# Optimization experiments

Measured on AMD Instinct MI355X. Metric: run time of the kernel, lower is better.

Reference implementation:

```python
import jax, jax.numpy as jnp
import numpy as np

N, L, D = 32768, 15, 256
VOCAB, SCORE_MAX = 27, 100


def setup_inputs() -> dict:
    key = jax.random.key(0)
    ks = jax.random.split(key, 16)
    inp = {
        'words': jax.random.randint(ks[0], (N, L), 0, VOCAB, dtype=jnp.int32),
        'rows': jax.random.randint(ks[1], (N,), 0, L, dtype=jnp.int32),
        'cols': jax.random.randint(ks[2], (N,), 0, L, dtype=jnp.int32),
        'dirs': jax.random.randint(ks[3], (N,), 0, 2, dtype=jnp.int32),
        'scores': jax.random.randint(ks[4], (N,), 0, 150, dtype=jnp.int32),
        'letter_emb': jax.random.normal(ks[5], (VOCAB, D), jnp.float32),
        'positional': jax.random.normal(ks[6], (L, D), jnp.float32),
        'Wq': jax.random.normal(ks[7], (D, D), jnp.float32) / np.sqrt(D),
        'bq': jax.random.normal(ks[8], (D,), jnp.float32) * 0.01,
        'Wk': jax.random.normal(ks[9], (D, D), jnp.float32) / np.sqrt(D),
        'bk': jax.random.normal(ks[10], (D,), jnp.float32) * 0.01,
        'Wv': jax.random.normal(ks[11], (D, D), jnp.float32) / np.sqrt(D),
        'bv': jax.random.normal(ks[12], (D,), jnp.float32) * 0.01,
        'row_emb': jax.random.normal(ks[13], (L, D), jnp.float32),
        'col_emb': jax.random.normal(ks[14], (L, D), jnp.float32),
        'dir_emb': jax.random.normal(ks[15], (2, D), jnp.float32),
        'score_emb': jax.random.normal(jax.random.fold_in(key, 99), (SCORE_MAX, D), jnp.float32),
    }
    return inp


def reference(words, rows, cols, dirs, scores, letter_emb, positional, Wq, bq, Wk, bk, Wv, bv, row_emb, col_emb, dir_emb, score_emb):
    # WordEncoder: letter embedding + positional, then single-head self-attention, sum over positions
    emb = letter_emb[words] + positional[None, :, :]            # [N, L, D]
    q = emb @ Wq.T + bq                                          # [N, L, D]
    k = emb @ Wk.T + bk
    v = emb @ Wv.T + bv
    att = jax.nn.softmax(jnp.einsum('nld,nmd->nlm', q, k), axis=-1)  # [N, L, L]
    word = jnp.einsum('nlm,nmd->nd', att, v)                     # (att @ v).sum(axis=1) -> [N, D]
    # VectorEncoder
    vector = row_emb[rows] + col_emb[cols] + dir_emb[dirs]       # [N, D]
    # score embedding (clamped to score_max - 1)
    score_v = score_emb[jnp.minimum(scores, SCORE_MAX - 1)]      # [N, D]
    # original computes word_enc(move.word) twice (word + ordered) -> 2 * word
    return 2.0 * word + vector + score_v
```

## Files before the change

kernel.cpp:

```cpp
#include <hip/hip_runtime.h>
#include <hip/hip_bf16.h>

#define NMOV 32768
#define LW 15
#define DIM 256
#define NVOC 27
#define NR 405
#define GSH 408
#define MPB 16

__device__ __forceinline__ float b2f(unsigned short u) {
    return __uint_as_float(((unsigned int)u) << 16);
}

__device__ const unsigned char PAIR_LUT[120] = {
    0x00,
    0x10,0x11,
    0x20,0x21,0x22,
    0x30,0x31,0x32,0x33,
    0x40,0x41,0x42,0x43,0x44,
    0x50,0x51,0x52,0x53,0x54,0x55,
    0x60,0x61,0x62,0x63,0x64,0x65,0x66,
    0x70,0x71,0x72,0x73,0x74,0x75,0x76,0x77,
    0x80,0x81,0x82,0x83,0x84,0x85,0x86,0x87,0x88,
    0x90,0x91,0x92,0x93,0x94,0x95,0x96,0x97,0x98,0x99,
    0xA0,0xA1,0xA2,0xA3,0xA4,0xA5,0xA6,0xA7,0xA8,0xA9,0xAA,
    0xB0,0xB1,0xB2,0xB3,0xB4,0xB5,0xB6,0xB7,0xB8,0xB9,0xBA,0xBB,
    0xC0,0xC1,0xC2,0xC3,0xC4,0xC5,0xC6,0xC7,0xC8,0xC9,0xCA,0xCB,0xCC,
    0xD0,0xD1,0xD2,0xD3,0xD4,0xD5,0xD6,0xD7,0xD8,0xD9,0xDA,0xDB,0xDC,0xDD,
    0xE0,0xE1,0xE2,0xE3,0xE4,0xE5,0xE6,0xE7,0xE8,0xE9,0xEA,0xEB,0xEC,0xED,0xEE
};

__global__ __launch_bounds__(256) void qkv_gemm(
    const float* __restrict__ le, const float* __restrict__ pos,
    const float* __restrict__ Wq, const float* __restrict__ bq,
    const float* __restrict__ Wk, const float* __restrict__ bk,
    const float* __restrict__ Wv, const float* __restrict__ bv,
    float* __restrict__ QT, float* __restrict__ KT,
    __hip_bfloat16* __restrict__ VT)
{
    __shared__ float Ash[32][260];
    __shared__ float Bsh[256][69];
    const int t  = threadIdx.x;
    const int gx = blockIdx.x % 12;
    const int gy = blockIdx.x / 12;
    const int r0 = gy * 32;
    const int mat = gx >> 2;
    const int nb  = (gx & 3) * 64;
    const float* W  = (mat == 0) ? Wq : (mat == 1) ? Wk : Wv;
    const float* bb = (mat == 0) ? bq : (mat == 1) ? bk : bv;

    #pragma unroll
    for (int s = 0; s < 8; ++s) {
        int slot = s * 256 + t;
        int row = slot >> 6, q4 = slot & 63;
        int r = r0 + row;
        float4 v = make_float4(0.f, 0.f, 0.f, 0.f);
        if (r < NR) {
            int c = r / 15, l = r - c * 15;
            float4 lv = *(const float4*)&le[c * DIM + q4 * 4];
            float4 pv = *(const float4*)&pos[l * DIM + q4 * 4];
            v = make_float4(lv.x + pv.x, lv.y + pv.y, lv.z + pv.z, lv.w + pv.w);
        }
        *(float4*)&Ash[row][q4 * 4] = v;
    }
    #pragma unroll
    for (int s = 0; s < 16; ++s) {
        int slot = s * 256 + t;
        int row = slot >> 6, q4 = slot & 63;
        float4 w4 = *(const float4*)&W[(nb + row) * DIM + q4 * 4];
        Bsh[q4 * 4 + 0][row] = w4.x;
        Bsh[q4 * 4 + 1][row] = w4.y;
        Bsh[q4 * 4 + 2][row] = w4.z;
        Bsh[q4 * 4 + 3][row] = w4.w;
    }
    __syncthreads();

    const int tn = t & 63, tm = t >> 6;
    float acc[8];
    #pragma unroll
    for (int rr = 0; rr < 8; ++rr) acc[rr] = 0.f;

    #pragma unroll 4
    for (int kq = 0; kq < 64; ++kq) {
        float4 a4[8];
        #pragma unroll
        for (int rr = 0; rr < 8; ++rr)
            a4[rr] = *(const float4*)&Ash[tm * 8 + rr][kq * 4];
        float b0 = Bsh[kq * 4 + 0][tn];
        float b1 = Bsh[kq * 4 + 1][tn];
        float b2 = Bsh[kq * 4 + 2][tn];
        float b3 = Bsh[kq * 4 + 3][tn];
        #pragma unroll
        for (int rr = 0; rr < 8; ++rr)
            acc[rr] += a4[rr].x * b0 + a4[rr].y * b1 + a4[rr].z * b2 + a4[rr].w * b3;
    }

    const float bias = bb[nb + tn];
    const int dcol = nb + tn;
    #pragma unroll
    for (int rr = 0; rr < 8; ++rr) {
        int r = r0 + tm * 8 + rr;
        if (r < NR) {
            float v = acc[rr] + bias;
            if (mat == 0)      QT[r * DIM + dcol] = v;
            else if (mat == 1) KT[r * DIM + dcol] = v;
            else               VT[r * DIM + dcol] = __float2bfloat16(v);
        }
    }
}

__global__ __launch_bounds__(256) void h_matrix(
    const float* __restrict__ QT, const float* __restrict__ KT,
    float2* __restrict__ H)
{
    __shared__ float Qi[16][68], Ki[16][68], Qj[16][68], Kj[16][68];

    int rem = blockIdx.x, bi = 0, cnt = 26;
    while (rem >= cnt) { rem -= cnt; ++bi; --cnt; }
    const int bj = bi + rem;
    const int i0 = bi * 16, j0 = bj * 16;
    const int t = threadIdx.x;
    const int ti = t >> 4, tj = t & 15;

    float acc_ij = 0.f, acc_ji = 0.f;

    for (int k0 = 0; k0 < DIM; k0 += 64) {
        #pragma unroll
        for (int s = 0; s < 4; ++s) {
            int slot = s * 256 + t;
            int tile = slot >> 8;
            int r    = (slot >> 4) & 15;
            int c4   = slot & 15;
            int grow = (tile < 2) ? (i0 + r) : (j0 + r);
            const float* src = (tile == 0 || tile == 2) ? QT : KT;
            float4 v = (grow < NR)
                ? *(const float4*)&src[grow * DIM + k0 + c4 * 4]
                : make_float4(0.f, 0.f, 0.f, 0.f);
            float* dst = (tile == 0) ? &Qi[r][c4 * 4]
                       : (tile == 1) ? &Ki[r][c4 * 4]
                       : (tile == 2) ? &Qj[r][c4 * 4] : &Kj[r][c4 * 4];
            *(float4*)dst = v;
        }
        __syncthreads();
        #pragma unroll 4
        for (int k = 0; k < 64; k += 4) {
            float4 qi = *(const float4*)&Qi[ti][k];
            float4 kj = *(const float4*)&Kj[tj][k];
            float4 qj = *(const float4*)&Qj[ti][k];
            float4 ki = *(const float4*)&Ki[tj][k];
            acc_ij += qi.x * kj.x + qi.y * kj.y + qi.z * kj.z + qi.w * kj.w;
            acc_ji += qj.x * ki.x + qj.y * ki.y + qj.z * ki.z + qj.w * ki.w;
        }
        __syncthreads();
    }

    Qi[ti][tj] = acc_ij;
    Ki[ti][tj] = acc_ji;
    __syncthreads();
    const float t_ij = Qi[tj][ti];
    const float t_ji = Ki[tj][ti];

    const int i1 = i0 + ti, j1 = j0 + tj;
    if (i1 < NR && j1 < NR) H[i1 * GSH + j1] = make_float2(acc_ij, t_ji);
    const int i2 = j0 + ti, j2 = i0 + tj;
    if (i2 < NR && j2 < NR) H[i2 * GSH + j2] = make_float2(acc_ji, t_ij);
}

__global__ __launch_bounds__(256) void moves_kernel(
    const int* __restrict__ words, const int* __restrict__ rowsI,
    const int* __restrict__ colsI, const int* __restrict__ dirsI,
    const int* __restrict__ scoresI,
    const float2* __restrict__ H, const __hip_bfloat16* __restrict__ VT,
    const float* __restrict__ row_emb, const float* __restrict__ col_emb,
    const float* __restrict__ dir_emb, const float* __restrict__ score_emb,
    float* __restrict__ out)
{
    __shared__ float S[MPB][LW][17];
    __shared__ int   rIdx[MPB][16];
    __shared__ float csum[MPB][16];
    const int base = blockIdx.x * MPB;
    const int t  = threadIdx.x;
    const int w  = t >> 6;
    const int ln = t & 63;
    const int hw = t >> 5;
    const int j  = t & 31;

    if (ln < 60) {
        int mvl = ln / 15, row = ln - mvl * 15;
        int mv = w * 4 + mvl;
        rIdx[mv][row] = words[(base + mv) * LW + row] * LW + row;
    }
    __builtin_amdgcn_wave_barrier();

    const int mv0 = hw * 2, mv1 = mv0 + 1;
    float2 h0[4], h1[4];
    int ll[4], mm[4];
    #pragma unroll
    for (int k = 0; k < 4; ++k) {
        int p = j + 32 * k;
        if (p < 120) {
            int lm = PAIR_LUT[p];
            ll[k] = lm >> 4; mm[k] = lm & 15;
            h0[k] = H[(size_t)rIdx[mv0][ll[k]] * GSH + rIdx[mv0][mm[k]]];
            h1[k] = H[(size_t)rIdx[mv1][ll[k]] * GSH + rIdx[mv1][mm[k]]];
        }
    }
    #pragma unroll
    for (int k = 0; k < 4; ++k) {
        int p = j + 32 * k;
        if (p < 120) {
            S[mv0][ll[k]][mm[k]] = h0[k].x;
            S[mv0][mm[k]][ll[k]] = h0[k].y;
            S[mv1][ll[k]][mm[k]] = h1[k].x;
            S[mv1][mm[k]][ll[k]] = h1[k].y;
        }
    }
    __builtin_amdgcn_wave_barrier();

    if (ln < 60) {
        int mvl = ln / 15, row = ln - mvl * 15;
        int mv = w * 4 + mvl;
        float s[LW];
        #pragma unroll
        for (int m = 0; m < LW; ++m) s[m] = S[mv][row][m];
        float mx = s[0];
        #pragma unroll
        for (int m = 1; m < LW; ++m) mx = fmaxf(mx, s[m]);
        float sum = 0.f;
        #pragma unroll
        for (int m = 0; m < LW; ++m) { s[m] = __expf(s[m] - mx); sum += s[m]; }
        float inv = 1.0f / sum;
        #pragma unroll
        for (int m = 0; m < LW; ++m) S[mv][row][m] = s[m] * inv;
    }
    __builtin_amdgcn_wave_barrier();

    if (ln < 60) {
        int mvl = ln / 15, col = ln - mvl * 15;
        int mv = w * 4 + mvl;
        float acc = 0.f;
        #pragma unroll
        for (int l = 0; l < LW; ++l) acc += S[mv][l][col];
        csum[mv][col] = acc;
    }
    __builtin_amdgcn_wave_barrier();

    const int d0 = ln * 4;
    const unsigned short* VT16 = (const unsigned short*)VT;
    #pragma unroll 1
    for (int s2 = 0; s2 < 4; ++s2) {
        const int i = w * 4 + s2;
        const int n = base + i;
        float4 re = *(const float4*)&row_emb[rowsI[n] * DIM + d0];
        float4 ce = *(const float4*)&col_emb[colsI[n] * DIM + d0];
        float4 de = *(const float4*)&dir_emb[dirsI[n] * DIM + d0];
        float4 se = *(const float4*)&score_emb[min(scoresI[n], 99) * DIM + d0];
        ushort4 va[8];
        #pragma unroll
        for (int m = 0; m < 8; ++m)
            va[m] = *(const ushort4*)(VT16 + (size_t)rIdx[i][m] * DIM + d0);
        float wx = 0.f, wy = 0.f, wz = 0.f, ww = 0.f;
        #pragma unroll
        for (int m = 0; m < 8; ++m) {
            float c = csum[i][m];
            wx += c * b2f(va[m].x); wy += c * b2f(va[m].y);
            wz += c * b2f(va[m].z); ww += c * b2f(va[m].w);
        }
        ushort4 vb[7];
        #pragma unroll
        for (int m = 0; m < 7; ++m)
            vb[m] = *(const ushort4*)(VT16 + (size_t)rIdx[i][8 + m] * DIM + d0);
        #pragma unroll
        for (int m = 0; m < 7; ++m) {
            float c = csum[i][8 + m];
            wx += c * b2f(vb[m].x); wy += c * b2f(vb[m].y);
            wz += c * b2f(vb[m].z); ww += c * b2f(vb[m].w);
        }
        float4 res;
        res.x = 2.f * wx + re.x + ce.x + de.x + se.x;
        res.y = 2.f * wy + re.y + ce.y + de.y + se.y;
        res.z = 2.f * wz + re.z + ce.z + de.z + se.z;
        res.w = 2.f * ww + re.w + ce.w + de.w + se.w;
        *(float4*)&out[(size_t)n * DIM + d0] = res;
    }
}

extern "C" void kernel_launch(void* const* d_in, const int* in_sizes, int n_in,
                              void* d_out, int out_size, void* d_ws, size_t ws_size,
                              hipStream_t stream)
{
    const int*   words      = (const int*)d_in[0];
    const int*   rowsI      = (const int*)d_in[1];
    const int*   colsI      = (const int*)d_in[2];
    const int*   dirsI      = (const int*)d_in[3];
    const int*   scoresI    = (const int*)d_in[4];
    const float* letter_emb = (const float*)d_in[5];
    const float* positional = (const float*)d_in[6];
    const float* Wq         = (const float*)d_in[7];
    const float* bq         = (const float*)d_in[8];
    const float* Wk         = (const float*)d_in[9];
    const float* bk         = (const float*)d_in[10];
    const float* Wv         = (const float*)d_in[11];
    const float* bv         = (const float*)d_in[12];
    const float* row_emb    = (const float*)d_in[13];
    const float* col_emb    = (const float*)d_in[14];
    const float* dir_emb    = (const float*)d_in[15];
    const float* score_emb  = (const float*)d_in[16];
    float* out = (float*)d_out;

    float*  QT = (float*)d_ws;
    float*  KT = QT + NR * DIM;
    float2* Hm = (float2*)(KT + NR * DIM);
    __hip_bfloat16* VT = (__hip_bfloat16*)((char*)Hm + (size_t)NR * GSH * sizeof(float2));

    qkv_gemm<<<156, 256, 0, stream>>>(letter_emb, positional, Wq, bq, Wk, bk,
                                      Wv, bv, QT, KT, VT);
    h_matrix<<<351, 256, 0, stream>>>(QT, KT, Hm);
    moves_kernel<<<NMOV / MPB, 256, 0, stream>>>(words, rowsI, colsI, dirsI,
                                                 scoresI, Hm, VT, row_emb,
                                                 col_emb, dir_emb, score_emb,
                                                 out);
}
```

Before: 68.10 us.

## Shrink QKV GEMM tiles for more blocks; stage move metadata in LDS

The QKV projection kernel now uses 16x16 output tiles with one output per thread across 1248 blocks instead of 32x64 tiles across 156 blocks. It also drops the transposed weight store into shared memory, so the small GEMM spreads over more compute units and has less per-block setup. Separately, the moves kernel loads row, col, dir and clamped score indices once into shared memory instead of each thread reading them from global memory. The trade-off is that every smaller GEMM block reloads full 256-wide rows of activations and weights, which adds redundant traffic.

```diff
diff --git a/kernel.cpp b/kernel.cpp
--- a/kernel.cpp
+++ b/kernel.cpp
@@ -39,74 +39,51 @@
     float* __restrict__ QT, float* __restrict__ KT,
     __hip_bfloat16* __restrict__ VT)
 {
-    __shared__ float Ash[32][260];
-    __shared__ float Bsh[256][69];
+    __shared__ float Ash[16][260];
+    __shared__ float Bsh[16][260];
     const int t  = threadIdx.x;
-    const int gx = blockIdx.x % 12;
-    const int gy = blockIdx.x / 12;
-    const int r0 = gy * 32;
-    const int mat = gx >> 2;
-    const int nb  = (gx & 3) * 64;
+    const int bx = blockIdx.x % 48;
+    const int by = blockIdx.x / 48;
+    const int r0 = by * 16;
+    const int mat = bx >> 4;
+    const int nb  = (bx & 15) * 16;
     const float* W  = (mat == 0) ? Wq : (mat == 1) ? Wk : Wv;
     const float* bb = (mat == 0) ? bq : (mat == 1) ? bk : bv;
 
     #pragma unroll
-    for (int s = 0; s < 8; ++s) {
+    for (int s = 0; s < 4; ++s) {
         int slot = s * 256 + t;
         int row = slot >> 6, q4 = slot & 63;
         int r = r0 + row;
-        float4 v = make_float4(0.f, 0.f, 0.f, 0.f);
+        float4 va = make_float4(0.f, 0.f, 0.f, 0.f);
         if (r < NR) {
             int c = r / 15, l = r - c * 15;
             float4 lv = *(const float4*)&le[c * DIM + q4 * 4];
             float4 pv = *(const float4*)&pos[l * DIM + q4 * 4];
-            v = make_float4(lv.x + pv.x, lv.y + pv.y, lv.z + pv.z, lv.w + pv.w);
-        }
-        *(float4*)&Ash[row][q4 * 4] = v;
-    }
-    #pragma unroll
-    for (int s = 0; s < 16; ++s) {
-        int slot = s * 256 + t;
-        int row = slot >> 6, q4 = slot & 63;
-        float4 w4 = *(const float4*)&W[(nb + row) * DIM + q4 * 4];
-        Bsh[q4 * 4 + 0][row] = w4.x;
-        Bsh[q4 * 4 + 1][row] = w4.y;
-        Bsh[q4 * 4 + 2][row] = w4.z;
-        Bsh[q4 * 4 + 3][row] = w4.w;
+            va = make_float4(lv.x + pv.x, lv.y + pv.y, lv.z + pv.z, lv.w + pv.w);
+        }
+        *(float4*)&Ash[row][q4 * 4] = va;
+        float4 vb = *(const float4*)&W[(nb + row) * DIM + q4 * 4];
+        *(float4*)&Bsh[row][q4 * 4] = vb;
     }
     __syncthreads();
 
-    const int tn = t & 63, tm = t >> 6;
-    float acc[8];
-    #pragma unroll
-    for (int rr = 0; rr < 8; ++rr) acc[rr] = 0.f;
-
-    #pragma unroll 4
-    for (int kq = 0; kq < 64; ++kq) {
-        float4 a4[8];
-        #pragma unroll
-        for (int rr = 0; rr < 8; ++rr)
-            a4[rr] = *(const float4*)&Ash[tm * 8 + rr][kq * 4];
-        float b0 = Bsh[kq * 4 + 0][tn];
-        float b1 = Bsh[kq * 4 + 1][tn];
-        float b2 = Bsh[kq * 4 + 2][tn];
-        float b3 = Bsh[kq * 4 + 3][tn];
-        #pragma unroll
-        for (int rr = 0; rr < 8; ++rr)
-            acc[rr] += a4[rr].x * b0 + a4[rr].y * b1 + a4[rr].z * b2 + a4[rr].w * b3;
-    }
-
-    const float bias = bb[nb + tn];
-    const int dcol = nb + tn;
-    #pragma unroll
-    for (int rr = 0; rr < 8; ++rr) {
-        int r = r0 + tm * 8 + rr;
-        if (r < NR) {
-            float v = acc[rr] + bias;
-            if (mat == 0)      QT[r * DIM + dcol] = v;
-            else if (mat == 1) KT[r * DIM + dcol] = v;
-            else               VT[r * DIM + dcol] = __float2bfloat16(v);
-        }
+    const int tj = t & 15, ti = t >> 4;
+    float acc = 0.f;
+    #pragma unroll 8
+    for (int k = 0; k < DIM; k += 4) {
+        float4 a = *(const float4*)&Ash[ti][k];
+        float4 b = *(const float4*)&Bsh[tj][k];
+        acc += a.x * b.x + a.y * b.y + a.z * b.z + a.w * b.w;
+    }
+
+    const int r = r0 + ti;
+    if (r < NR) {
+        float v = acc + bb[nb + tj];
+        int dcol = nb + tj;
+        if (mat == 0)      QT[r * DIM + dcol] = v;
+        else if (mat == 1) KT[r * DIM + dcol] = v;
+        else               VT[r * DIM + dcol] = __float2bfloat16(v);
     }
 }
 
@@ -179,6 +156,7 @@
     __shared__ float S[MPB][LW][17];
     __shared__ int   rIdx[MPB][16];
     __shared__ float csum[MPB][16];
+    __shared__ int   meta[MPB][4];
     const int base = blockIdx.x * MPB;
     const int t  = threadIdx.x;
     const int w  = t >> 6;
@@ -190,6 +168,13 @@
         int mvl = ln / 15, row = ln - mvl * 15;
         int mv = w * 4 + mvl;
         rIdx[mv][row] = words[(base + mv) * LW + row] * LW + row;
+    }
+    if (ln < 16) {
+        int mvl = ln >> 2, f = ln & 3;
+        int n = base + w * 4 + mvl;
+        int v = (f == 0) ? rowsI[n] : (f == 1) ? colsI[n]
+              : (f == 2) ? dirsI[n] : min(scoresI[n], 99);
+        meta[w * 4 + mvl][f] = v;
     }
     __builtin_amdgcn_wave_barrier();
 
@@ -252,10 +237,10 @@
     for (int s2 = 0; s2 < 4; ++s2) {
         const int i = w * 4 + s2;
         const int n = base + i;
-        float4 re = *(const float4*)&row_emb[rowsI[n] * DIM + d0];
-        float4 ce = *(const float4*)&col_emb[colsI[n] * DIM + d0];
-        float4 de = *(const float4*)&dir_emb[dirsI[n] * DIM + d0];
-        float4 se = *(const float4*)&score_emb[min(scoresI[n], 99) * DIM + d0];
+        float4 re = *(const float4*)&row_emb[meta[i][0] * DIM + d0];
+        float4 ce = *(const float4*)&col_emb[meta[i][1] * DIM + d0];
+        float4 de = *(const float4*)&dir_emb[meta[i][2] * DIM + d0];
+        float4 se = *(const float4*)&score_emb[meta[i][3] * DIM + d0];
         ushort4 va[8];
         #pragma unroll
         for (int m = 0; m < 8; ++m)
@@ -314,8 +299,8 @@
     float2* Hm = (float2*)(KT + NR * DIM);
     __hip_bfloat16* VT = (__hip_bfloat16*)((char*)Hm + (size_t)NR * GSH * sizeof(float2));
 
-    qkv_gemm<<<156, 256, 0, stream>>>(letter_emb, positional, Wq, bq, Wk, bk,
-                                      Wv, bv, QT, KT, VT);
+    qkv_gemm<<<26 * 48, 256, 0, stream>>>(letter_emb, positional, Wq, bq, Wk, bk,
+                                          Wv, bv, QT, KT, VT);
     h_matrix<<<351, 256, 0, stream>>>(QT, KT, Hm);
     moves_kernel<<<NMOV / MPB, 256, 0, stream>>>(words, rowsI, colsI, dirsI,
                                                  scoresI, Hm, VT, row_emb,
```

Measured after the change: 63.20 us. 7.2% less time.
